# Performance work log

Hardware: AMD Instinct MI355X
Metric: run time of the kernel (lower is better)

The kernel has to match this reference:

```python
import jax, jax.numpy as jnp
import numpy as np

H = 8  # number of heads


def setup_inputs() -> dict:
    key = jax.random.key(0)
    ks = jax.random.split(key, 7)
    B, L, D = 4, 2048, 512
    dh = D // H
    s = 1.0 / np.sqrt(D).astype(np.float32)
    return {
        "q": jax.random.normal(ks[0], (B, L, D), jnp.float32),
        "k": jax.random.normal(ks[1], (B, L, D), jnp.float32),
        "v": jax.random.normal(ks[2], (B, L, D), jnp.float32),
        "Wq": jax.random.normal(ks[3], (D, D), jnp.float32) * s,
        "Wk": jax.random.normal(ks[4], (D, D), jnp.float32) * s,
        "Wv": jax.random.normal(ks[5], (D, D), jnp.float32) * s,
        "E": jax.random.normal(ks[6], (L, dh), jnp.float32) * s,
    }


def _skew(QE):
    # QE: [B, H, L, L] -> pad one column on the left, reshape to [B,H,L+1,L],
    # drop the first row: the classic Music Transformer skewing trick.
    B, h, L, M = QE.shape
    padded = jnp.pad(QE, ((0, 0), (0, 0), (0, 0), (1, 0)))
    return padded.reshape(B, h, M + 1, L)[:, :, 1:, :]


def reference(q, k, v, Wq, Wk, Wv, E):
    B, L, D = q.shape
    dh = D // H

    def heads(x, W):
        return jnp.einsum('bld,de->ble', x, W).reshape(B, L, H, dh).transpose(0, 2, 1, 3)

    qh = heads(q, Wq)  # [B,H,L,dh]
    kh = heads(k, Wk)
    vh = heads(v, Wv)

    QE = jnp.einsum('bhld,md->bhlm', qh, E)      # [B,H,L,L]
    Srel = _skew(QE)                             # [B,H,L,L]
    QKt = jnp.einsum('bhld,bhmd->bhlm', qh, kh)  # [B,H,L,L]

    # NOTE: original divides AFTER softmax (faithful to source).
    attn = jax.nn.softmax(QKt + Srel, axis=-1) / float(np.sqrt(dh))
    out = jnp.einsum('bhlm,bhmd->bhld', attn, vh)
    return out.transpose(0, 2, 1, 3).reshape(B, L, D)
```

## Files before the change

kernel.cpp:

```cpp
#include <hip/hip_runtime.h>
#include <hip/hip_bf16.h>
#include <math.h>

typedef _Float16 f16;
typedef __attribute__((ext_vector_type(8))) _Float16 f16x8;
typedef __attribute__((ext_vector_type(4))) _Float16 f16x4;
typedef __attribute__((ext_vector_type(4))) float f32x4;

namespace {
constexpr int B = 4, L = 2048, D = 512, NH = 8, DH = 64;
constexpr int HALF = 1024;
}

__global__ __launch_bounds__(256)
void ecast_kernel(const float* __restrict__ E, f16* __restrict__ Ef) {
    int i4 = (blockIdx.x * 256 + threadIdx.x) * 4;
    float4 x = *(const float4*)(E + i4);
    *(f16x4*)(Ef + i4) = (f16x4){(f16)x.x, (f16)x.y, (f16)x.z, (f16)x.w};
}

__global__ __launch_bounds__(256)
void wtrans_kernel(const float* __restrict__ Wq, const float* __restrict__ Wk,
                   const float* __restrict__ Wv, f16* __restrict__ Wt) {
    __shared__ f16 Ws[64 * 65];
    const int sel = blockIdx.z;
    const float* W = (sel == 0) ? Wq : (sel == 1) ? Wk : Wv;
    f16* Wo = Wt + (size_t)sel * D * D;
    const int k0 = blockIdx.x * 64, n0 = blockIdx.y * 64;
    const int t = threadIdx.x;
#pragma unroll
    for (int i = 0; i < 16; ++i) {
        int idx = 256 * i + t;
        int r = idx >> 6, c = idx & 63;
        Ws[r * 65 + c] = (f16)W[(size_t)(k0 + r) * D + n0 + c];
    }
    __syncthreads();
    const int c = t >> 2, kseg = t & 3;
    f16x8 r0, r1;
#pragma unroll
    for (int j = 0; j < 8; ++j) r0[j] = Ws[(kseg * 16 + j) * 65 + c];
#pragma unroll
    for (int j = 0; j < 8; ++j) r1[j] = Ws[(kseg * 16 + 8 + j) * 65 + c];
    f16* o = Wo + (size_t)(n0 + c) * D + k0 + kseg * 16;
    *(f16x8*)o = r0;
    *(f16x8*)(o + 8) = r1;
}

__global__ __launch_bounds__(256, 4)
void proj_gemm(const float* __restrict__ q, const float* __restrict__ k,
               const float* __restrict__ v, const f16* __restrict__ Wt,
               f16* __restrict__ Qf, f16* __restrict__ Kf, f16* __restrict__ Vtf) {
    __shared__ f16 As[128 * 72];
    __shared__ f16 Bs[64 * 72];
    const int bx = blockIdx.x, by = blockIdx.y;
    const int sel = by >> 3, h = by & 7;
    const int m0 = bx * 128;
    const float* X = (sel == 0) ? q : (sel == 1) ? k : v;
    const f16* Bt = Wt + (size_t)sel * D * D + (size_t)h * 64 * D;
    const int t = threadIdx.x, wid = t >> 6, lane = t & 63;
    const int quad = lane >> 4, col = lane & 15;
    const int mw = wid * 32;

    f32x4 acc[2][4];
#pragma unroll
    for (int i = 0; i < 2; ++i)
#pragma unroll
        for (int j = 0; j < 4; ++j) acc[i][j] = (f32x4){0.f, 0.f, 0.f, 0.f};

    float4 xa[8];
    f16x8 breg[2];
    auto loadG = [&](int k0) {
#pragma unroll
        for (int i = 0; i < 8; ++i) {
            int idx = 256 * i + t;
            int r = idx >> 4, c4 = idx & 15;
            xa[i] = *(const float4*)(X + (size_t)(m0 + r) * D + k0 + c4 * 4);
        }
#pragma unroll
        for (int i = 0; i < 2; ++i) {
            int idx = 256 * i + t;
            int r = idx >> 3, ch = idx & 7;
            breg[i] = *(const f16x8*)(Bt + (size_t)r * D + k0 + ch * 8);
        }
    };
    auto storeL = [&]() {
#pragma unroll
        for (int i = 0; i < 8; ++i) {
            int idx = 256 * i + t;
            int r = idx >> 4, c4 = idx & 15;
            *(f16x4*)(As + r * 72 + c4 * 4) =
                (f16x4){(f16)xa[i].x, (f16)xa[i].y, (f16)xa[i].z, (f16)xa[i].w};
        }
#pragma unroll
        for (int i = 0; i < 2; ++i) {
            int idx = 256 * i + t;
            int r = idx >> 3, ch = idx & 7;
            *(f16x8*)(Bs + r * 72 + ch * 8) = breg[i];
        }
    };

    loadG(0);
    for (int k0 = 0; k0 < D; k0 += 64) {
        __syncthreads();
        storeL();
        __syncthreads();
        if (k0 + 64 < D) loadG(k0 + 64);
#pragma unroll
        for (int ks = 0; ks < 2; ++ks) {
            f16x8 af[2], bf[4];
#pragma unroll
            for (int mt = 0; mt < 2; ++mt)
                af[mt] = *(const f16x8*)(As + (mw + mt * 16 + col) * 72 + quad * 8 + ks * 32);
#pragma unroll
            for (int nt = 0; nt < 4; ++nt)
                bf[nt] = *(const f16x8*)(Bs + (nt * 16 + col) * 72 + quad * 8 + ks * 32);
#pragma unroll
            for (int mt = 0; mt < 2; ++mt)
#pragma unroll
                for (int nt = 0; nt < 4; ++nt)
                    acc[mt][nt] = __builtin_amdgcn_mfma_f32_16x16x32_f16(af[mt], bf[nt], acc[mt][nt], 0, 0, 0);
        }
    }

    if (sel < 2) {
        f16* Y = (sel == 0) ? Qf : Kf;
#pragma unroll
        for (int mt = 0; mt < 2; ++mt)
#pragma unroll
            for (int nt = 0; nt < 4; ++nt)
#pragma unroll
                for (int reg = 0; reg < 4; ++reg) {
                    int m = m0 + mw + mt * 16 + quad * 4 + reg;
                    int bb = m >> 11, l = m & 2047, d = nt * 16 + col;
                    Y[((size_t)(bb * NH + h) * L + l) * DH + d] = (f16)acc[mt][nt][reg];
                }
    } else {
        __syncthreads();
        f16* Cs = As;
#pragma unroll
        for (int mt = 0; mt < 2; ++mt)
#pragma unroll
            for (int nt = 0; nt < 4; ++nt)
#pragma unroll
                for (int reg = 0; reg < 4; ++reg) {
                    int d = nt * 16 + col;
                    int lc = mw + mt * 16 + quad * 4 + reg;
                    Cs[d * 136 + lc] = (f16)acc[mt][nt][reg];
                }
        __syncthreads();
        const int dd = t >> 2, seg = t & 3;
        const int bb = m0 >> 11, l0 = m0 & 2047;
        f16* Yv = Vtf + ((size_t)(bb * NH + h) * DH + dd) * L + l0 + seg * 32;
#pragma unroll
        for (int j = 0; j < 4; ++j)
            *(f16x8*)(Yv + j * 8) = *(const f16x8*)(Cs + dd * 136 + seg * 32 + j * 8);
    }
}

__global__ __launch_bounds__(256)
void attn_kernel(const f16* __restrict__ Qf, const f16* __restrict__ Kf,
                 const f16* __restrict__ Vtf, const f16* __restrict__ Ef,
                 f16* __restrict__ Opart, float* __restrict__ Mpart,
                 float* __restrict__ Spart) {
    __shared__ f16 KS[2][64 * 72];
    __shared__ f16 VS[2][64 * 72];
    __shared__ f16 Pbuf[4][16 * 72];

    const int t = threadIdx.x, wid = t >> 6, lane = t & 63;
    const int quad = lane >> 4, col = lane & 15;
    const int l0w = blockIdx.x * 64 + wid * 16;
    const int h = blockIdx.y;
    const int bb = blockIdx.z >> 1, half = blockIdx.z & 1;
    const int c0beg = half * HALF, c0end = c0beg + HALF;
    const size_t head = (size_t)(bb * NH + h) * (size_t)(L * DH);
    const f16* qf = Qf + head;
    const f16* kf = Kf + head;
    const f16* vt = Vtf + head;
    f16* Pw = Pbuf[wid];

    f16x8 qF[2], qS[2];
    {
        const int m = l0w + col;
        const int mS = min(m + 1, L - 1);
#pragma unroll
        for (int ks = 0; ks < 2; ++ks) {
            const int off = quad * 8 + ks * 32;
            qF[ks] = *(const f16x8*)(qf + (size_t)m * DH + off);
            qS[ks] = *(const f16x8*)(qf + (size_t)mS * DH + off);
        }
    }

    f16x8 kreg[2], vreg[2];
    auto loadKV = [&](int c0) {
#pragma unroll
        for (int i = 0; i < 2; ++i) {
            int idx = 256 * i + t;
            int r = idx >> 3, ch = idx & 7;
            kreg[i] = *(const f16x8*)(kf + (size_t)(c0 + r) * DH + ch * 8);
            vreg[i] = *(const f16x8*)(vt + (size_t)r * L + c0 + ch * 8);
        }
    };

    f32x4 O[4];
#pragma unroll
    for (int i = 0; i < 4; ++i) O[i] = (f32x4){0.f, 0.f, 0.f, 0.f};
    float mrow[4] = {-1e30f, -1e30f, -1e30f, -1e30f};
    float srow[4] = {0.f, 0.f, 0.f, 0.f};

    loadKV(c0beg);
    int buf = 0;
    for (int c0 = c0beg; c0 < c0end; c0 += 64, buf ^= 1) {
        f16* KSb = KS[buf];
        f16* VSb = VS[buf];
#pragma unroll
        for (int i = 0; i < 2; ++i) {
            int idx = 256 * i + t;
            int r = idx >> 3, ch = idx & 7;
            *(f16x8*)(KSb + r * 72 + ch * 8) = kreg[i];
            *(f16x8*)(VSb + r * 72 + ch * 8) = vreg[i];
        }
        __syncthreads();
        if (c0 + 64 < c0end) loadKV(c0 + 64);

        const int d0 = c0 - l0w;

        f32x4 S[4];
#pragma unroll
        for (int ns = 0; ns < 4; ++ns) {
            S[ns] = (f32x4){0.f, 0.f, 0.f, 0.f};
#pragma unroll
            for (int ks = 0; ks < 2; ++ks) {
                f16x8 bh = *(const f16x8*)(KSb + (ns * 16 + col) * 72 + quad * 8 + ks * 32);
                S[ns] = __builtin_amdgcn_mfma_f32_16x16x32_f16(qF[ks], bh, S[ns], 0, 0, 0);
            }
        }

        const bool doA = (d0 <= 15);
        const bool doB = (d0 >= -61);
#pragma unroll 1
        for (int pass = 0; pass < 2; ++pass) {
            if ((pass == 0 && !doA) || (pass == 1 && !doB)) continue;
            const int jbase = (pass == 0) ? (d0 + L - 16) : (d0 - 17);
            f32x4 G[5];
#pragma unroll
            for (int g = 0; g < 5; ++g) {
                int er = min(max(jbase + g * 16 + col, 0), L - 1);
                G[g] = (f32x4){0.f, 0.f, 0.f, 0.f};
                const size_t eb = (size_t)er * DH + quad * 8;
#pragma unroll
                for (int ks = 0; ks < 2; ++ks) {
                    f16x8 e8 = *(const f16x8*)(Ef + eb + ks * 32);
                    G[g] = __builtin_amdgcn_mfma_f32_16x16x32_f16(
                               (pass == 0) ? qF[ks] : qS[ks], e8, G[g], 0, 0, 0);
                }
            }
#pragma unroll
            for (int reg = 0; reg < 4; ++reg) {
                const int r  = quad * 4 + reg;
                const int jj = col - r + 15;
                const int src = quad * 16 + (jj & 15);
#pragma unroll
                for (int ns = 0; ns < 4; ++ns) {
                    float v0 = __shfl(G[ns][reg], src, 64);
                    float v1 = __shfl(G[ns + 1][reg], src, 64);
                    float val = (jj < 16) ? v0 : v1;
                    const int rel = d0 + ns * 16 + col - r;
                    const bool use = (pass == 0) ? (rel <= 0) : (rel >= 2);
                    if (use) S[ns][reg] += val;
                }
            }
        }

#pragma unroll
        for (int reg = 0; reg < 4; ++reg) {
            float tm = fmaxf(fmaxf(S[0][reg], S[1][reg]), fmaxf(S[2][reg], S[3][reg]));
#pragma unroll
            for (int msk = 1; msk < 16; msk <<= 1)
                tm = fmaxf(tm, __shfl_xor(tm, msk, 16));
            const float mnew  = fmaxf(mrow[reg], tm);
            const float alpha = __expf(mrow[reg] - mnew);
            float p[4], ps = 0.f;
#pragma unroll
            for (int ns = 0; ns < 4; ++ns) { p[ns] = __expf(S[ns][reg] - mnew); ps += p[ns]; }
#pragma unroll
            for (int msk = 1; msk < 16; msk <<= 1)
                ps += __shfl_xor(ps, msk, 16);
            srow[reg] = srow[reg] * alpha + ps;
            mrow[reg] = mnew;
            const int r = quad * 4 + reg;
#pragma unroll
            for (int ns = 0; ns < 4; ++ns) {
                O[ns][reg] *= alpha;
                Pw[r * 72 + ns * 16 + col] = (f16)p[ns];
            }
        }

        f16x8 pA[2];
        pA[0] = *(const f16x8*)(Pw + col * 72 + quad * 8);
        pA[1] = *(const f16x8*)(Pw + col * 72 + 32 + quad * 8);
#pragma unroll
        for (int ns = 0; ns < 4; ++ns) {
#pragma unroll
            for (int ks = 0; ks < 2; ++ks) {
                f16x8 v8 = *(const f16x8*)(VSb + (ns * 16 + col) * 72 + quad * 8 + ks * 32);
                O[ns] = __builtin_amdgcn_mfma_f32_16x16x32_f16(pA[ks], v8, O[ns], 0, 0, 0);
            }
        }
    }

#pragma unroll
    for (int reg = 0; reg < 4; ++reg) {
        const int l = l0w + quad * 4 + reg;
        const size_t row = ((size_t)(half * B + bb) * NH + h) * L + l;
        f16* o = Opart + row * DH;
#pragma unroll
        for (int ns = 0; ns < 4; ++ns)
            o[ns * 16 + col] = (f16)O[ns][reg];
        if (col == 0) {
            Mpart[row] = mrow[reg];
            Spart[row] = srow[reg];
        }
    }
}

__global__ __launch_bounds__(256)
void combine_kernel(const f16* __restrict__ Opart, const float* __restrict__ Mpart,
                    const float* __restrict__ Spart, float* __restrict__ out) {
    const int gid = blockIdx.x * 256 + threadIdx.x;
    const int row = gid >> 3;
    const int dseg = (gid & 7) * 8;
    const int bb = row >> 14;
    const int rem = row & 16383;
    const int h = rem >> 11, l = rem & 2047;
    const int HSTRIDE = B * NH * L;

    const float m0 = Mpart[row], m1 = Mpart[row + HSTRIDE];
    const float s0 = Spart[row], s1 = Spart[row + HSTRIDE];
    const float m = fmaxf(m0, m1);
    const float e0 = __expf(m0 - m), e1 = __expf(m1 - m);
    const float inv = 1.0f / ((s0 * e0 + s1 * e1) * 8.0f);
    const float w0 = e0 * inv, w1 = e1 * inv;

    f16x8 o0 = *(const f16x8*)(Opart + (size_t)row * DH + dseg);
    f16x8 o1 = *(const f16x8*)(Opart + ((size_t)row + HSTRIDE) * DH + dseg);
    float* o = out + ((size_t)bb * L + l) * D + h * DH + dseg;
    float4 lo, hi;
    lo.x = (float)o0[0] * w0 + (float)o1[0] * w1;
    lo.y = (float)o0[1] * w0 + (float)o1[1] * w1;
    lo.z = (float)o0[2] * w0 + (float)o1[2] * w1;
    lo.w = (float)o0[3] * w0 + (float)o1[3] * w1;
    hi.x = (float)o0[4] * w0 + (float)o1[4] * w1;
    hi.y = (float)o0[5] * w0 + (float)o1[5] * w1;
    hi.z = (float)o0[6] * w0 + (float)o1[6] * w1;
    hi.w = (float)o0[7] * w0 + (float)o1[7] * w1;
    *(float4*)o = lo;
    *(float4*)(o + 4) = hi;
}

extern "C" void kernel_launch(void* const* d_in, const int* in_sizes, int n_in,
                              void* d_out, int out_size, void* d_ws, size_t ws_size,
                              hipStream_t stream) {
    const float* q  = (const float*)d_in[0];
    const float* k  = (const float*)d_in[1];
    const float* v  = (const float*)d_in[2];
    const float* Wq = (const float*)d_in[3];
    const float* Wk = (const float*)d_in[4];
    const float* Wv = (const float*)d_in[5];
    const float* E  = (const float*)d_in[6];
    float* out = (float*)d_out;

    const size_t plane = (size_t)B * NH * L * DH;
    f16* Qf  = (f16*)d_ws;
    f16* Kfp = Qf + plane;
    f16* Vtf = Kfp + plane;
    f16* Wt  = Vtf + plane;
    f16* Ef  = Wt + (size_t)3 * D * D;
    f16* Opart = Ef + (size_t)L * DH;
    float* Mpart = (float*)(Opart + 2 * plane);
    float* Spart = Mpart + (size_t)2 * B * NH * L;

    ecast_kernel<<<L * DH / 1024, 256, 0, stream>>>(E, Ef);
    wtrans_kernel<<<dim3(8, 8, 3), 256, 0, stream>>>(Wq, Wk, Wv, Wt);
    proj_gemm<<<dim3(64, 24), 256, 0, stream>>>(q, k, v, Wt, Qf, Kfp, Vtf);
    attn_kernel<<<dim3(L / 64, NH, B * 2), 256, 0, stream>>>(Qf, Kfp, Vtf, Ef,
                                                             Opart, Mpart, Spart);
    combine_kernel<<<(B * NH * L * DH / 8) / 256, 256, 0, stream>>>(Opart, Mpart, Spart, out);
}
```

Measured before the change: 399.3 us.

## Read K/V directly from global in attention and halve skew shuffles

Removes the double-buffered shared-memory staging of K and V tiles and the per-iteration block barrier. Each wave now reads its K and V MFMA operands straight from global memory and relies on the caches for reuse across the four waves. The relative-position skew also changes: the G tiles are computed one at a time, and the source lane picks which tile to send, so only one shuffle is needed per element instead of two. This cuts shared-memory use, barriers and register pressure, but the global loads are no longer prefetched, so their latency is exposed and the same data is fetched redundantly by each wave.

After: 516.9 us. 29.5% more time.

```diff
diff --git a/kernel.cpp b/kernel.cpp
--- a/kernel.cpp
+++ b/kernel.cpp
@@ -107,18 +107,18 @@
         if (k0 + 64 < D) loadG(k0 + 64);
 #pragma unroll
         for (int ks = 0; ks < 2; ++ks) {
-            f16x8 af[2], bf[4];
+            f16x8 af[2], bfr[4];
 #pragma unroll
             for (int mt = 0; mt < 2; ++mt)
                 af[mt] = *(const f16x8*)(As + (mw + mt * 16 + col) * 72 + quad * 8 + ks * 32);
 #pragma unroll
             for (int nt = 0; nt < 4; ++nt)
-                bf[nt] = *(const f16x8*)(Bs + (nt * 16 + col) * 72 + quad * 8 + ks * 32);
+                bfr[nt] = *(const f16x8*)(Bs + (nt * 16 + col) * 72 + quad * 8 + ks * 32);
 #pragma unroll
             for (int mt = 0; mt < 2; ++mt)
 #pragma unroll
                 for (int nt = 0; nt < 4; ++nt)
-                    acc[mt][nt] = __builtin_amdgcn_mfma_f32_16x16x32_f16(af[mt], bf[nt], acc[mt][nt], 0, 0, 0);
+                    acc[mt][nt] = __builtin_amdgcn_mfma_f32_16x16x32_f16(af[mt], bfr[nt], acc[mt][nt], 0, 0, 0);
         }
     }
 
@@ -162,8 +162,6 @@
                  const f16* __restrict__ Vtf, const f16* __restrict__ Ef,
                  f16* __restrict__ Opart, float* __restrict__ Mpart,
                  float* __restrict__ Spart) {
-    __shared__ f16 KS[2][64 * 72];
-    __shared__ f16 VS[2][64 * 72];
     __shared__ f16 Pbuf[4][16 * 72];
 
     const int t = threadIdx.x, wid = t >> 6, lane = t & 63;
@@ -190,47 +188,23 @@
         }
     }
 
-    f16x8 kreg[2], vreg[2];
-    auto loadKV = [&](int c0) {
-#pragma unroll
-        for (int i = 0; i < 2; ++i) {
-            int idx = 256 * i + t;
-            int r = idx >> 3, ch = idx & 7;
-            kreg[i] = *(const f16x8*)(kf + (size_t)(c0 + r) * DH + ch * 8);
-            vreg[i] = *(const f16x8*)(vt + (size_t)r * L + c0 + ch * 8);
-        }
-    };
-
     f32x4 O[4];
 #pragma unroll
     for (int i = 0; i < 4; ++i) O[i] = (f32x4){0.f, 0.f, 0.f, 0.f};
     float mrow[4] = {-1e30f, -1e30f, -1e30f, -1e30f};
     float srow[4] = {0.f, 0.f, 0.f, 0.f};
 
-    loadKV(c0beg);
-    int buf = 0;
-    for (int c0 = c0beg; c0 < c0end; c0 += 64, buf ^= 1) {
-        f16* KSb = KS[buf];
-        f16* VSb = VS[buf];
-#pragma unroll
-        for (int i = 0; i < 2; ++i) {
-            int idx = 256 * i + t;
-            int r = idx >> 3, ch = idx & 7;
-            *(f16x8*)(KSb + r * 72 + ch * 8) = kreg[i];
-            *(f16x8*)(VSb + r * 72 + ch * 8) = vreg[i];
-        }
-        __syncthreads();
-        if (c0 + 64 < c0end) loadKV(c0 + 64);
-
+    for (int c0 = c0beg; c0 < c0end; c0 += 64) {
         const int d0 = c0 - l0w;
 
         f32x4 S[4];
 #pragma unroll
         for (int ns = 0; ns < 4; ++ns) {
             S[ns] = (f32x4){0.f, 0.f, 0.f, 0.f};
+            const size_t kb = (size_t)(c0 + ns * 16 + col) * DH + quad * 8;
 #pragma unroll
             for (int ks = 0; ks < 2; ++ks) {
-                f16x8 bh = *(const f16x8*)(KSb + (ns * 16 + col) * 72 + quad * 8 + ks * 32);
+                f16x8 bh = *(const f16x8*)(kf + kb + ks * 32);
                 S[ns] = __builtin_amdgcn_mfma_f32_16x16x32_f16(qF[ks], bh, S[ns], 0, 0, 0);
             }
         }
@@ -241,33 +215,33 @@
         for (int pass = 0; pass < 2; ++pass) {
             if ((pass == 0 && !doA) || (pass == 1 && !doB)) continue;
             const int jbase = (pass == 0) ? (d0 + L - 16) : (d0 - 17);
-            f32x4 G[5];
-#pragma unroll
-            for (int g = 0; g < 5; ++g) {
+            auto calcG = [&](int g) -> f32x4 {
                 int er = min(max(jbase + g * 16 + col, 0), L - 1);
-                G[g] = (f32x4){0.f, 0.f, 0.f, 0.f};
+                f32x4 G = (f32x4){0.f, 0.f, 0.f, 0.f};
                 const size_t eb = (size_t)er * DH + quad * 8;
 #pragma unroll
                 for (int ks = 0; ks < 2; ++ks) {
                     f16x8 e8 = *(const f16x8*)(Ef + eb + ks * 32);
-                    G[g] = __builtin_amdgcn_mfma_f32_16x16x32_f16(
-                               (pass == 0) ? qF[ks] : qS[ks], e8, G[g], 0, 0, 0);
+                    G = __builtin_amdgcn_mfma_f32_16x16x32_f16(
+                            (pass == 0) ? qF[ks] : qS[ks], e8, G, 0, 0, 0);
                 }
-            }
-#pragma unroll
-            for (int reg = 0; reg < 4; ++reg) {
-                const int r  = quad * 4 + reg;
-                const int jj = col - r + 15;
-                const int src = quad * 16 + (jj & 15);
-#pragma unroll
-                for (int ns = 0; ns < 4; ++ns) {
-                    float v0 = __shfl(G[ns][reg], src, 64);
-                    float v1 = __shfl(G[ns + 1][reg], src, 64);
-                    float val = (jj < 16) ? v0 : v1;
+                return G;
+            };
+            f32x4 Ga = calcG(0), Gb;
+#pragma unroll
+            for (int ns = 0; ns < 4; ++ns) {
+                Gb = calcG(ns + 1);
+#pragma unroll
+                for (int reg = 0; reg < 4; ++reg) {
+                    const int r = quad * 4 + reg;
+                    const float tmp = (col >= 15 - r) ? Ga[reg] : Gb[reg];
+                    const int src = quad * 16 + ((col - r + 15) & 15);
+                    const float val = __shfl(tmp, src, 64);
                     const int rel = d0 + ns * 16 + col - r;
                     const bool use = (pass == 0) ? (rel <= 0) : (rel >= 2);
                     if (use) S[ns][reg] += val;
                 }
+                Ga = Gb;
             }
         }
 
@@ -300,9 +274,10 @@
         pA[1] = *(const f16x8*)(Pw + col * 72 + 32 + quad * 8);
 #pragma unroll
         for (int ns = 0; ns < 4; ++ns) {
+            const size_t vb = (size_t)(ns * 16 + col) * L + c0 + quad * 8;
 #pragma unroll
             for (int ks = 0; ks < 2; ++ks) {
-                f16x8 v8 = *(const f16x8*)(VSb + (ns * 16 + col) * 72 + quad * 8 + ks * 32);
+                f16x8 v8 = *(const f16x8*)(vt + vb + ks * 32);
                 O[ns] = __builtin_amdgcn_mfma_f32_16x16x32_f16(pA[ks], v8, O[ns], 0, 0, 0);
             }
         }
```

## Compute softmax row sums via MFMA with ones vector; single-buffer K/V LDS

Applied to the files above, without the earlier changes.

The attention kernel no longer sums the exponentials with shuffle reductions. It multiplies the fp16 P tile by a vector of ones with two extra MFMAs per tile, which removes four xor-shuffle steps per row register. The K/V shared buffers also go from double to single buffering, with an extra barrier before each store, which frees LDS but adds a sync per tile. The row sum is now taken over the fp16-rounded probabilities, which matches what is multiplied into V. The GEMM change is only a variable rename.

Measured after the change: 395.2 us. No clear change (-1.0%).

```diff
diff --git a/kernel.cpp b/kernel.cpp
--- a/kernel.cpp
+++ b/kernel.cpp
@@ -107,18 +107,18 @@
         if (k0 + 64 < D) loadG(k0 + 64);
 #pragma unroll
         for (int ks = 0; ks < 2; ++ks) {
-            f16x8 af[2], bf[4];
+            f16x8 af[2], bfr[4];
 #pragma unroll
             for (int mt = 0; mt < 2; ++mt)
                 af[mt] = *(const f16x8*)(As + (mw + mt * 16 + col) * 72 + quad * 8 + ks * 32);
 #pragma unroll
             for (int nt = 0; nt < 4; ++nt)
-                bf[nt] = *(const f16x8*)(Bs + (nt * 16 + col) * 72 + quad * 8 + ks * 32);
+                bfr[nt] = *(const f16x8*)(Bs + (nt * 16 + col) * 72 + quad * 8 + ks * 32);
 #pragma unroll
             for (int mt = 0; mt < 2; ++mt)
 #pragma unroll
                 for (int nt = 0; nt < 4; ++nt)
-                    acc[mt][nt] = __builtin_amdgcn_mfma_f32_16x16x32_f16(af[mt], bf[nt], acc[mt][nt], 0, 0, 0);
+                    acc[mt][nt] = __builtin_amdgcn_mfma_f32_16x16x32_f16(af[mt], bfr[nt], acc[mt][nt], 0, 0, 0);
         }
     }
 
@@ -162,8 +162,8 @@
                  const f16* __restrict__ Vtf, const f16* __restrict__ Ef,
                  f16* __restrict__ Opart, float* __restrict__ Mpart,
                  float* __restrict__ Spart) {
-    __shared__ f16 KS[2][64 * 72];
-    __shared__ f16 VS[2][64 * 72];
+    __shared__ f16 KfS[64 * 72];
+    __shared__ f16 VfS[64 * 72];
     __shared__ f16 Pbuf[4][16 * 72];
 
     const int t = threadIdx.x, wid = t >> 6, lane = t & 63;
@@ -190,6 +190,10 @@
         }
     }
 
+    f16x8 onesf;
+#pragma unroll
+    for (int j = 0; j < 8; ++j) onesf[j] = (f16)1.0f;
+
     f16x8 kreg[2], vreg[2];
     auto loadKV = [&](int c0) {
 #pragma unroll
@@ -201,23 +205,21 @@
         }
     };
 
-    f32x4 O[4];
+    f32x4 O[4], Osum;
 #pragma unroll
     for (int i = 0; i < 4; ++i) O[i] = (f32x4){0.f, 0.f, 0.f, 0.f};
+    Osum = (f32x4){0.f, 0.f, 0.f, 0.f};
     float mrow[4] = {-1e30f, -1e30f, -1e30f, -1e30f};
-    float srow[4] = {0.f, 0.f, 0.f, 0.f};
 
     loadKV(c0beg);
-    int buf = 0;
-    for (int c0 = c0beg; c0 < c0end; c0 += 64, buf ^= 1) {
-        f16* KSb = KS[buf];
-        f16* VSb = VS[buf];
+    for (int c0 = c0beg; c0 < c0end; c0 += 64) {
+        __syncthreads();
 #pragma unroll
         for (int i = 0; i < 2; ++i) {
             int idx = 256 * i + t;
             int r = idx >> 3, ch = idx & 7;
-            *(f16x8*)(KSb + r * 72 + ch * 8) = kreg[i];
-            *(f16x8*)(VSb + r * 72 + ch * 8) = vreg[i];
+            *(f16x8*)(KfS + r * 72 + ch * 8) = kreg[i];
+            *(f16x8*)(VfS + r * 72 + ch * 8) = vreg[i];
         }
         __syncthreads();
         if (c0 + 64 < c0end) loadKV(c0 + 64);
@@ -230,7 +232,7 @@
             S[ns] = (f32x4){0.f, 0.f, 0.f, 0.f};
 #pragma unroll
             for (int ks = 0; ks < 2; ++ks) {
-                f16x8 bh = *(const f16x8*)(KSb + (ns * 16 + col) * 72 + quad * 8 + ks * 32);
+                f16x8 bh = *(const f16x8*)(KfS + (ns * 16 + col) * 72 + quad * 8 + ks * 32);
                 S[ns] = __builtin_amdgcn_mfma_f32_16x16x32_f16(qF[ks], bh, S[ns], 0, 0, 0);
             }
         }
@@ -279,19 +281,13 @@
                 tm = fmaxf(tm, __shfl_xor(tm, msk, 16));
             const float mnew  = fmaxf(mrow[reg], tm);
             const float alpha = __expf(mrow[reg] - mnew);
-            float p[4], ps = 0.f;
-#pragma unroll
-            for (int ns = 0; ns < 4; ++ns) { p[ns] = __expf(S[ns][reg] - mnew); ps += p[ns]; }
-#pragma unroll
-            for (int msk = 1; msk < 16; msk <<= 1)
-                ps += __shfl_xor(ps, msk, 16);
-            srow[reg] = srow[reg] * alpha + ps;
             mrow[reg] = mnew;
+            Osum[reg] *= alpha;
             const int r = quad * 4 + reg;
 #pragma unroll
             for (int ns = 0; ns < 4; ++ns) {
                 O[ns][reg] *= alpha;
-                Pw[r * 72 + ns * 16 + col] = (f16)p[ns];
+                Pw[r * 72 + ns * 16 + col] = (f16)__expf(S[ns][reg] - mnew);
             }
         }
 
@@ -302,10 +298,12 @@
         for (int ns = 0; ns < 4; ++ns) {
 #pragma unroll
             for (int ks = 0; ks < 2; ++ks) {
-                f16x8 v8 = *(const f16x8*)(VSb + (ns * 16 + col) * 72 + quad * 8 + ks * 32);
+                f16x8 v8 = *(const f16x8*)(VfS + (ns * 16 + col) * 72 + quad * 8 + ks * 32);
                 O[ns] = __builtin_amdgcn_mfma_f32_16x16x32_f16(pA[ks], v8, O[ns], 0, 0, 0);
             }
         }
+        Osum = __builtin_amdgcn_mfma_f32_16x16x32_f16(pA[0], onesf, Osum, 0, 0, 0);
+        Osum = __builtin_amdgcn_mfma_f32_16x16x32_f16(pA[1], onesf, Osum, 0, 0, 0);
     }
 
 #pragma unroll
@@ -318,7 +316,7 @@
             o[ns * 16 + col] = (f16)O[ns][reg];
         if (col == 0) {
             Mpart[row] = mrow[reg];
-            Spart[row] = srow[reg];
+            Spart[row] = Osum[reg];
         }
     }
 }
```
